# Performance work log

Hardware: AMD Instinct MI355X
Metric: run time of the kernel (lower is better)

## Reference

```python
import jax, jax.numpy as jnp
import numpy as np

N_HEAD = 8
D_K = 32
D_IN = 512
B, T = 16, 1024


def setup_inputs() -> dict:
    key = jax.random.key(0)
    ks = jax.random.split(key, 8)
    q = jax.random.normal(ks[0], (B, T, D_IN), dtype=jnp.float32)
    k = jax.random.normal(ks[1], (B, T, D_IN), dtype=jnp.float32)
    v = jax.random.normal(ks[2], (B, T, D_IN), dtype=jnp.float32)
    pad_mask = jax.random.randint(ks[3], (B, T), 0, 2).astype(jnp.bool_)
    std = np.sqrt(2.0 / D_K).astype(np.float32)
    W_q = jax.random.normal(ks[4], (N_HEAD * D_K, D_IN), dtype=jnp.float32) * std
    b_q = jax.random.normal(ks[5], (N_HEAD * D_K,), dtype=jnp.float32) * 0.01
    W_k = jax.random.normal(ks[6], (N_HEAD * D_K, D_IN), dtype=jnp.float32) * std
    b_k = jax.random.normal(ks[7], (N_HEAD * D_K,), dtype=jnp.float32) * 0.01
    return {"q": q, "k": k, "v": v, "pad_mask": pad_mask,
            "W_q": W_q, "b_q": b_q, "W_k": W_k, "b_k": b_k}


def reference(q, k, v, pad_mask, W_q, b_q, W_k, b_k):
    # NOTE: faithful to the torch module -- queries AND keys are projected
    # from v; the q, k inputs only supply shapes.
    b, t, d_in = v.shape
    h, dk = N_HEAD, D_K
    dh = d_in // h  # per-head value dim
    temperature = jnp.asarray(np.power(dk, 0.5), dtype=v.dtype)

    qh = (jnp.einsum('btd,ed->bte', v, W_q) + b_q).reshape(b, t, h, dk)
    kh = (jnp.einsum('btd,ed->bte', v, W_k) + b_k).reshape(b, t, h, dk)

    # scores: [b, h, q, k]
    scores = jnp.einsum('bqhd,bkhd->bhqk', qh, kh) / temperature
    scores = jnp.where(pad_mask[:, None, None, :], jnp.asarray(-1000.0, scores.dtype), scores)
    attn = jax.nn.softmax(scores, axis=-1)

    # value heads: split last dim into h chunks -> [b, t, h, dh]
    vh = v.reshape(b, t, h, dh)
    out = jnp.einsum('bhqk,bkhd->bhqd', attn, vh)

    # match torch output layout: output [h, b, t, dh], attn [h, b, t, t]
    output = jnp.transpose(out, (1, 0, 2, 3))
    attn_out = jnp.transpose(attn, (1, 0, 2, 3))
    return output, attn_out
```

## Files before the change

### kernel.cpp

```cpp
#include <hip/hip_runtime.h>
#include <math.h>

#define NHEAD 8
#define DK 32
#define DIN 512
#define BB 16
#define TT 1024
#define DH 64
#define EE 256
#define OUT_OFF (NHEAD*BB*TT*DH)
#define INVTEMP 0.17677669529663687f

__global__ __launch_bounds__(256)
void mask_repack_kernel(const unsigned char* __restrict__ raw,
                        unsigned char* __restrict__ norm)
{
    __shared__ int sflag;
    const int t = threadIdx.x;
    if (t == 0) sflag = 0;
    __syncthreads();

    int f = 0;
    for (int i = t; i < BB*TT/4; i += 256) {
        uchar4 b4 = reinterpret_cast<const uchar4*>(raw)[i];
        f |= (int)b4.y | (int)b4.z | (int)b4.w;
    }
    if (f) atomicOr(&sflag, 1);
    __syncthreads();

    if (sflag) {
        for (int i = t; i < BB*TT; i += 256)
            norm[i] = raw[i] ? 1 : 0;
    } else {
        const int* ri = reinterpret_cast<const int*>(raw);
        for (int i = t; i < BB*TT; i += 256)
            norm[i] = ri[i] ? 1 : 0;
    }
}

__global__ __launch_bounds__(256)
void proj_kernel(const float* __restrict__ v,
                 const float* __restrict__ Wq, const float* __restrict__ bq,
                 const float* __restrict__ Wk, const float* __restrict__ bk,
                 float* __restrict__ qh, float* __restrict__ kh)
{
    __shared__ float As[16][132];
    __shared__ float Bs[16][132];

    const int m0 = blockIdx.x * 128;
    const int nb = blockIdx.y;
    const bool isQ = (nb < 2);
    const float* __restrict__ W    = isQ ? (Wq + (size_t)nb*128*DIN)
                                         : (Wk + (size_t)(nb-2)*128*DIN);
    const float* __restrict__ bias = isQ ? (bq + nb*128) : (bk + (nb-2)*128);
    float* __restrict__ C          = isQ ? qh : kh;
    const int   c0    = (nb & 1) * 128;
    const float scale = isQ ? INVTEMP : 1.0f;

    const int t  = threadIdx.x;
    const int tx = t & 15, ty = t >> 4;

    float acc[8][8];
    #pragma unroll
    for (int i = 0; i < 8; ++i)
        #pragma unroll
        for (int j = 0; j < 8; ++j) acc[i][j] = 0.0f;

    for (int k0 = 0; k0 < DIN; k0 += 16) {
        #pragma unroll
        for (int l = 0; l < 2; ++l) {
            int idx = t + l*256;
            int row = idx >> 2, c4 = idx & 3;
            float4 a = *reinterpret_cast<const float4*>(
                &v[(size_t)(m0+row)*DIN + k0 + c4*4]);
            As[c4*4+0][row] = a.x; As[c4*4+1][row] = a.y;
            As[c4*4+2][row] = a.z; As[c4*4+3][row] = a.w;
            float4 b = *reinterpret_cast<const float4*>(
                &W[(size_t)row*DIN + k0 + c4*4]);
            Bs[c4*4+0][row] = b.x; Bs[c4*4+1][row] = b.y;
            Bs[c4*4+2][row] = b.z; Bs[c4*4+3][row] = b.w;
        }
        __syncthreads();
        #pragma unroll
        for (int kk = 0; kk < 16; ++kk) {
            float a[8], b[8];
            *reinterpret_cast<float4*>(&a[0]) = *reinterpret_cast<const float4*>(&As[kk][ty*8]);
            *reinterpret_cast<float4*>(&a[4]) = *reinterpret_cast<const float4*>(&As[kk][ty*8+4]);
            *reinterpret_cast<float4*>(&b[0]) = *reinterpret_cast<const float4*>(&Bs[kk][tx*8]);
            *reinterpret_cast<float4*>(&b[4]) = *reinterpret_cast<const float4*>(&Bs[kk][tx*8+4]);
            #pragma unroll
            for (int i = 0; i < 8; ++i)
                #pragma unroll
                for (int j = 0; j < 8; ++j)
                    acc[i][j] += a[i]*b[j];
        }
        __syncthreads();
    }

    #pragma unroll
    for (int i = 0; i < 8; ++i) {
        float4 o0, o1;
        o0.x = (acc[i][0] + bias[tx*8+0]) * scale;
        o0.y = (acc[i][1] + bias[tx*8+1]) * scale;
        o0.z = (acc[i][2] + bias[tx*8+2]) * scale;
        o0.w = (acc[i][3] + bias[tx*8+3]) * scale;
        o1.x = (acc[i][4] + bias[tx*8+4]) * scale;
        o1.y = (acc[i][5] + bias[tx*8+5]) * scale;
        o1.z = (acc[i][6] + bias[tx*8+6]) * scale;
        o1.w = (acc[i][7] + bias[tx*8+7]) * scale;
        size_t base = (size_t)(m0 + ty*8 + i)*EE + c0 + tx*8;
        *reinterpret_cast<float4*>(&C[base])   = o0;
        *reinterpret_cast<float4*>(&C[base+4]) = o1;
    }
}

#define PVSTEP(PC, VV)                                                                          \
    acc[0][0] += p0.PC*VV.x; acc[0][1] += p0.PC*VV.y; acc[0][2] += p0.PC*VV.z; acc[0][3] += p0.PC*VV.w; \
    acc[1][0] += p1.PC*VV.x; acc[1][1] += p1.PC*VV.y; acc[1][2] += p1.PC*VV.z; acc[1][3] += p1.PC*VV.w; \
    acc[2][0] += p2.PC*VV.x; acc[2][1] += p2.PC*VV.y; acc[2][2] += p2.PC*VV.z; acc[2][3] += p2.PC*VV.w; \
    acc[3][0] += p3.PC*VV.x; acc[3][1] += p3.PC*VV.y; acc[3][2] += p3.PC*VV.z; acc[3][3] += p3.PC*VV.w;

__global__ __launch_bounds__(256)
void attn_kernel(const float* __restrict__ qh, const float* __restrict__ kh,
                 const float* __restrict__ v, const unsigned char* __restrict__ mask,
                 float* __restrict__ out)
{
    __shared__ float qhs[16][32];
    __shared__ float khsT[32][134];
    __shared__ float vhs[128][64];
    __shared__ float pbuf[16][132];
    __shared__ float obuf[4][16][64];

    const int q0   = blockIdx.x * 16;
    const int b    = blockIdx.y;
    const int h    = blockIdx.z;
    const int t    = threadIdx.x;
    const int lane = t & 63, w = t >> 6;
    const int k0l  = 2*lane;

    #pragma unroll
    for (int l = 0; l < 2; ++l) {
        int idx = t + l*256;
        int r = idx >> 5, d = idx & 31;
        qhs[r][d] = qh[(size_t)(b*TT + q0 + r)*EE + h*DK + d];
    }
    __syncthreads();

    const float* __restrict__ khb = kh + (size_t)b*TT*EE + h*DK;

    float s[4][16];

    #pragma unroll
    for (int c = 0; c < 8; ++c) {
        #pragma unroll
        for (int l = 0; l < 16; ++l) {
            int idx = t + 256*l;
            int d = idx & 31, k = idx >> 5;
            khsT[d][k] = khb[(size_t)(c*128 + k)*EE + d];
        }
        __syncthreads();

        float s0[4] = {0,0,0,0}, s1[4] = {0,0,0,0};
        #pragma unroll
        for (int dg = 0; dg < 8; ++dg) {
            float2 ka = *reinterpret_cast<const float2*>(&khsT[dg*4+0][k0l]);
            float2 kb = *reinterpret_cast<const float2*>(&khsT[dg*4+1][k0l]);
            float2 kc = *reinterpret_cast<const float2*>(&khsT[dg*4+2][k0l]);
            float2 kd = *reinterpret_cast<const float2*>(&khsT[dg*4+3][k0l]);
            #pragma unroll
            for (int rr = 0; rr < 4; ++rr) {
                float4 q4 = *reinterpret_cast<const float4*>(&qhs[4*w+rr][dg*4]);
                s0[rr] += q4.x*ka.x + q4.y*kb.x + q4.z*kc.x + q4.w*kd.x;
                s1[rr] += q4.x*ka.y + q4.y*kb.y + q4.z*kc.y + q4.w*kd.y;
            }
        }
        uchar2 mk = *reinterpret_cast<const uchar2*>(&mask[(size_t)b*TT + c*128 + k0l]);
        #pragma unroll
        for (int rr = 0; rr < 4; ++rr) {
            s[rr][2*c+0] = mk.x ? -1000.0f : s0[rr];
            s[rr][2*c+1] = mk.y ? -1000.0f : s1[rr];
        }
        __syncthreads();
    }

    #pragma unroll
    for (int rr = 0; rr < 4; ++rr) {
        float m = s[rr][0];
        #pragma unroll
        for (int j = 1; j < 16; ++j) m = fmaxf(m, s[rr][j]);
        #pragma unroll
        for (int o = 32; o >= 1; o >>= 1) m = fmaxf(m, __shfl_xor(m, o, 64));
        float l = 0.0f;
        #pragma unroll
        for (int j = 0; j < 16; ++j) { float e = __expf(s[rr][j] - m); s[rr][j] = e; l += e; }
        #pragma unroll
        for (int o = 32; o >= 1; o >>= 1) l += __shfl_xor(l, o, 64);
        float inv = 1.0f / l;
        #pragma unroll
        for (int j = 0; j < 16; ++j) s[rr][j] *= inv;
    }

    float* __restrict__ attnout = out + OUT_OFF + (size_t)((h*BB + b)*TT + q0)*TT;
    #pragma unroll
    for (int rr = 0; rr < 4; ++rr) {
        float* __restrict__ rowp = attnout + (size_t)(4*w+rr)*TT;
        #pragma unroll
        for (int c = 0; c < 8; ++c) {
            *reinterpret_cast<float2*>(&rowp[c*128 + k0l]) =
                make_float2(s[rr][2*c], s[rr][2*c+1]);
        }
    }

    float acc[4][4];
    #pragma unroll
    for (int i = 0; i < 4; ++i)
        #pragma unroll
        for (int j = 0; j < 4; ++j) acc[i][j] = 0.0f;

    const float* __restrict__ vb = v + (size_t)b*TT*DIN + h*DH;
    const int rg = lane >> 4, dg = lane & 15;

    #pragma unroll
    for (int vc = 0; vc < 8; ++vc) {
        __syncthreads();
        #pragma unroll
        for (int l = 0; l < 8; ++l) {
            int idx = t + 256*l;
            int row = idx >> 4, c4 = idx & 15;
            *reinterpret_cast<float4*>(&vhs[row][c4*4]) =
                *reinterpret_cast<const float4*>(&vb[(size_t)(vc*128+row)*DIN + c4*4]);
        }
        #pragma unroll
        for (int rr = 0; rr < 4; ++rr) {
            *reinterpret_cast<float2*>(&pbuf[4*w+rr][k0l]) =
                make_float2(s[rr][2*vc], s[rr][2*vc+1]);
        }
        __syncthreads();

        #pragma unroll
        for (int kk = 0; kk < 32; kk += 4) {
            const int kbase = w*32 + kk;
            float4 p0 = *reinterpret_cast<const float4*>(&pbuf[rg*4+0][kbase]);
            float4 p1 = *reinterpret_cast<const float4*>(&pbuf[rg*4+1][kbase]);
            float4 p2 = *reinterpret_cast<const float4*>(&pbuf[rg*4+2][kbase]);
            float4 p3 = *reinterpret_cast<const float4*>(&pbuf[rg*4+3][kbase]);
            { float4 vv = *reinterpret_cast<const float4*>(&vhs[kbase+0][dg*4]); PVSTEP(x, vv) }
            { float4 vv = *reinterpret_cast<const float4*>(&vhs[kbase+1][dg*4]); PVSTEP(y, vv) }
            { float4 vv = *reinterpret_cast<const float4*>(&vhs[kbase+2][dg*4]); PVSTEP(z, vv) }
            { float4 vv = *reinterpret_cast<const float4*>(&vhs[kbase+3][dg*4]); PVSTEP(w, vv) }
        }
    }

    #pragma unroll
    for (int rr = 0; rr < 4; ++rr) {
        *reinterpret_cast<float4*>(&obuf[w][rg*4+rr][dg*4]) =
            make_float4(acc[rr][0], acc[rr][1], acc[rr][2], acc[rr][3]);
    }
    __syncthreads();
    {
        int r = t >> 4, c4 = t & 15;
        float4 r0 = *reinterpret_cast<const float4*>(&obuf[0][r][c4*4]);
        float4 r1 = *reinterpret_cast<const float4*>(&obuf[1][r][c4*4]);
        float4 r2 = *reinterpret_cast<const float4*>(&obuf[2][r][c4*4]);
        float4 r3 = *reinterpret_cast<const float4*>(&obuf[3][r][c4*4]);
        float4 o;
        o.x = r0.x + r1.x + r2.x + r3.x;
        o.y = r0.y + r1.y + r2.y + r3.y;
        o.z = r0.z + r1.z + r2.z + r3.z;
        o.w = r0.w + r1.w + r2.w + r3.w;
        *reinterpret_cast<float4*>(
            &out[(size_t)((h*BB + b)*TT + q0 + r)*DH + c4*4]) = o;
    }
}

extern "C" void kernel_launch(void* const* d_in, const int* in_sizes, int n_in,
                              void* d_out, int out_size, void* d_ws, size_t ws_size,
                              hipStream_t stream)
{
    const float* v  = (const float*)d_in[2];
    const unsigned char* mask_raw = (const unsigned char*)d_in[3];
    const float* Wq = (const float*)d_in[4];
    const float* bq = (const float*)d_in[5];
    const float* Wk = (const float*)d_in[6];
    const float* bk = (const float*)d_in[7];
    float* out = (float*)d_out;

    float* qh = (float*)d_ws;
    float* kh = qh + (size_t)BB*TT*EE;
    unsigned char* mask_norm =
        (unsigned char*)(kh + (size_t)BB*TT*EE);

    mask_repack_kernel<<<1, 256, 0, stream>>>(mask_raw, mask_norm);

    dim3 pgrid(128, 4);
    proj_kernel<<<pgrid, 256, 0, stream>>>(v, Wq, bq, Wk, bk, qh, kh);

    dim3 agrid(TT/16, BB, NHEAD);
    attn_kernel<<<agrid, 256, 0, stream>>>(qh, kh, v, mask_norm, out);
}
```

Baseline: 1.256 ms.

## Rewrite projection and attention on bf16 MFMA with split hi/lo precision

Replaces the scalar FP32 projection and attention kernels with MFMA bf16 versions. Inputs are split into hi/lo bf16 pairs so QK^T and the projection keep near-FP32 accuracy using three MFMAs. Weights are pre-scaled and converted, V is transposed to bf16, and P·V runs through a swizzled LDS buffer in bf16. The goal is to move the matmul FLOPs onto matrix cores, at the cost of extra conversion kernels and reduced precision in P·V.

```diff
diff --git a/kernel.cpp b/kernel.cpp
--- a/kernel.cpp
+++ b/kernel.cpp
@@ -8,8 +8,23 @@
 #define TT 1024
 #define DH 64
 #define EE 256
-#define OUT_OFF (NHEAD*BB*TT*DH)
+#define OUT_OFF ((size_t)NHEAD*BB*TT*DH)
 #define INVTEMP 0.17677669529663687f
+
+typedef short bf16x8 __attribute__((ext_vector_type(8)));
+typedef float f32x4  __attribute__((ext_vector_type(4)));
+
+__device__ __forceinline__ short f2bf(float f) {
+    union { float f; unsigned u; } c; c.f = f;
+    unsigned u = c.u;
+    unsigned r = (u + 0x7fffu + ((u >> 16) & 1u)) >> 16;
+    return (short)r;
+}
+__device__ __forceinline__ float bf2f(short s) {
+    union { unsigned u; float f; } c;
+    c.u = ((unsigned)(unsigned short)s) << 16;
+    return c.f;
+}
 
 __global__ __launch_bounds__(256)
 void mask_repack_kernel(const unsigned char* __restrict__ raw,
@@ -19,7 +34,6 @@
     const int t = threadIdx.x;
     if (t == 0) sflag = 0;
     __syncthreads();
-
     int f = 0;
     for (int i = t; i < BB*TT/4; i += 256) {
         uchar4 b4 = reinterpret_cast<const uchar4*>(raw)[i];
@@ -27,250 +41,226 @@
     }
     if (f) atomicOr(&sflag, 1);
     __syncthreads();
-
     if (sflag) {
-        for (int i = t; i < BB*TT; i += 256)
-            norm[i] = raw[i] ? 1 : 0;
+        for (int i = t; i < BB*TT; i += 256) norm[i] = raw[i] ? 1 : 0;
     } else {
         const int* ri = reinterpret_cast<const int*>(raw);
-        for (int i = t; i < BB*TT; i += 256)
-            norm[i] = ri[i] ? 1 : 0;
-    }
-}
-
-__global__ __launch_bounds__(256)
-void proj_kernel(const float* __restrict__ v,
-                 const float* __restrict__ Wq, const float* __restrict__ bq,
-                 const float* __restrict__ Wk, const float* __restrict__ bk,
-                 float* __restrict__ qh, float* __restrict__ kh)
-{
-    __shared__ float As[16][132];
-    __shared__ float Bs[16][132];
-
-    const int m0 = blockIdx.x * 128;
-    const int nb = blockIdx.y;
-    const bool isQ = (nb < 2);
-    const float* __restrict__ W    = isQ ? (Wq + (size_t)nb*128*DIN)
-                                         : (Wk + (size_t)(nb-2)*128*DIN);
-    const float* __restrict__ bias = isQ ? (bq + nb*128) : (bk + (nb-2)*128);
-    float* __restrict__ C          = isQ ? qh : kh;
-    const int   c0    = (nb & 1) * 128;
-    const float scale = isQ ? INVTEMP : 1.0f;
-
+        for (int i = t; i < BB*TT; i += 256) norm[i] = ri[i] ? 1 : 0;
+    }
+}
+
+__global__ __launch_bounds__(256)
+void conv_w_kernel(const float* __restrict__ Wq, const float* __restrict__ bq,
+                   const float* __restrict__ Wk, const float* __restrict__ bk,
+                   short* __restrict__ Whi, short* __restrict__ Wlo,
+                   float* __restrict__ bc)
+{
+    const int e = blockIdx.x;
+    const float sc = (e < 256) ? INVTEMP : 1.0f;
+    const float* src = (e < 256) ? (Wq + (size_t)e*DIN) : (Wk + (size_t)(e-256)*DIN);
+    for (int d = threadIdx.x; d < DIN; d += 256) {
+        float f = src[d] * sc;
+        short h = f2bf(f);
+        Whi[(size_t)e*DIN + d] = h;
+        Wlo[(size_t)e*DIN + d] = f2bf(f - bf2f(h));
+    }
+    if (threadIdx.x == 0)
+        bc[e] = ((e < 256) ? bq[e] : bk[e-256]) * sc;
+}
+
+__global__ __launch_bounds__(256)
+void conv_vt_kernel(const float* __restrict__ v, short* __restrict__ vT)
+{
+    __shared__ float tile[64][65];
+    const int t0 = blockIdx.x * 64;
+    const int b = blockIdx.y, h = blockIdx.z;
+    const int t = threadIdx.x;
+    #pragma unroll
+    for (int i = 0; i < 16; ++i) {
+        int idx = i*256 + t;
+        int r = idx >> 6, dd = idx & 63;
+        tile[dd][r] = v[((size_t)b*TT + t0 + r)*DIN + h*DH + dd];
+    }
+    __syncthreads();
+    const int d = t >> 2, seg = t & 3;
+    bf16x8 o0, o1;
+    #pragma unroll
+    for (int j = 0; j < 8; ++j) {
+        o0[j] = f2bf(tile[d][seg*16 + j]);
+        o1[j] = f2bf(tile[d][seg*16 + 8 + j]);
+    }
+    short* dst = vT + ((size_t)(b*NHEAD + h)*DH + d)*TT + t0 + seg*16;
+    *(bf16x8*)(dst)     = o0;
+    *(bf16x8*)(dst + 8) = o1;
+}
+
+__global__ __launch_bounds__(256)
+void proj_kernel(const float* __restrict__ v, const short* __restrict__ Whi,
+                 const short* __restrict__ Wlo, const float* __restrict__ bc,
+                 short* __restrict__ Phi, short* __restrict__ Plo)
+{
+    const int t = threadIdx.x;
+    const int lane = t & 63, w = t >> 6;
+    const int x = lane & 15, g = lane >> 4;
+    const int m0 = blockIdx.x * 64 + w * 16;
+    const int n0 = blockIdx.y * 64;
+
+    const float* arow = v + (size_t)(m0 + x) * DIN;
+    f32x4 acc[4];
+    #pragma unroll
+    for (int cc = 0; cc < 4; ++cc) {
+        acc[cc][0] = 0.f; acc[cc][1] = 0.f; acc[cc][2] = 0.f; acc[cc][3] = 0.f;
+    }
+
+    for (int d0 = 0; d0 < DIN; d0 += 32) {
+        float4 a0 = *(const float4*)(arow + d0 + g*8);
+        float4 a1 = *(const float4*)(arow + d0 + g*8 + 4);
+        float av[8] = {a0.x, a0.y, a0.z, a0.w, a1.x, a1.y, a1.z, a1.w};
+        bf16x8 ahi, alo;
+        #pragma unroll
+        for (int j = 0; j < 8; ++j) {
+            short hh = f2bf(av[j]);
+            ahi[j] = hh;
+            alo[j] = f2bf(av[j] - bf2f(hh));
+        }
+        #pragma unroll
+        for (int cc = 0; cc < 4; ++cc) {
+            size_t boff = (size_t)(n0 + cc*16 + x) * DIN + d0 + g*8;
+            bf16x8 bhi = *(const bf16x8*)(Whi + boff);
+            bf16x8 blo = *(const bf16x8*)(Wlo + boff);
+            acc[cc] = __builtin_amdgcn_mfma_f32_16x16x32_bf16(ahi, bhi, acc[cc], 0, 0, 0);
+            acc[cc] = __builtin_amdgcn_mfma_f32_16x16x32_bf16(alo, bhi, acc[cc], 0, 0, 0);
+            acc[cc] = __builtin_amdgcn_mfma_f32_16x16x32_bf16(ahi, blo, acc[cc], 0, 0, 0);
+        }
+    }
+
+    #pragma unroll
+    for (int cc = 0; cc < 4; ++cc) {
+        const int n = n0 + cc*16 + x;
+        const float bias = bc[n];
+        #pragma unroll
+        for (int r = 0; r < 4; ++r) {
+            const int m = m0 + g*4 + r;
+            float val = acc[cc][r] + bias;
+            short hh = f2bf(val);
+            Phi[(size_t)m*512 + n] = hh;
+            Plo[(size_t)m*512 + n] = f2bf(val - bf2f(hh));
+        }
+    }
+}
+
+__global__ __launch_bounds__(256)
+void attn_kernel(const short* __restrict__ Phi, const short* __restrict__ Plo,
+                 const short* __restrict__ vT, const unsigned char* __restrict__ mask,
+                 float* __restrict__ out)
+{
+    __shared__ short pbuf[16*1024];
+    __shared__ float redmax[4][4][4];
+    __shared__ float redsum[4][4][4];
+
+    const int q0 = blockIdx.x * 16;
+    const int b  = blockIdx.y;
+    const int h  = blockIdx.z;
     const int t  = threadIdx.x;
-    const int tx = t & 15, ty = t >> 4;
-
-    float acc[8][8];
-    #pragma unroll
-    for (int i = 0; i < 8; ++i)
-        #pragma unroll
-        for (int j = 0; j < 8; ++j) acc[i][j] = 0.0f;
-
-    for (int k0 = 0; k0 < DIN; k0 += 16) {
-        #pragma unroll
-        for (int l = 0; l < 2; ++l) {
-            int idx = t + l*256;
-            int row = idx >> 2, c4 = idx & 3;
-            float4 a = *reinterpret_cast<const float4*>(
-                &v[(size_t)(m0+row)*DIN + k0 + c4*4]);
-            As[c4*4+0][row] = a.x; As[c4*4+1][row] = a.y;
-            As[c4*4+2][row] = a.z; As[c4*4+3][row] = a.w;
-            float4 b = *reinterpret_cast<const float4*>(
-                &W[(size_t)row*DIN + k0 + c4*4]);
-            Bs[c4*4+0][row] = b.x; Bs[c4*4+1][row] = b.y;
-            Bs[c4*4+2][row] = b.z; Bs[c4*4+3][row] = b.w;
-        }
-        __syncthreads();
-        #pragma unroll
-        for (int kk = 0; kk < 16; ++kk) {
-            float a[8], b[8];
-            *reinterpret_cast<float4*>(&a[0]) = *reinterpret_cast<const float4*>(&As[kk][ty*8]);
-            *reinterpret_cast<float4*>(&a[4]) = *reinterpret_cast<const float4*>(&As[kk][ty*8+4]);
-            *reinterpret_cast<float4*>(&b[0]) = *reinterpret_cast<const float4*>(&Bs[kk][tx*8]);
-            *reinterpret_cast<float4*>(&b[4]) = *reinterpret_cast<const float4*>(&Bs[kk][tx*8+4]);
-            #pragma unroll
-            for (int i = 0; i < 8; ++i)
-                #pragma unroll
-                for (int j = 0; j < 8; ++j)
-                    acc[i][j] += a[i]*b[j];
-        }
-        __syncthreads();
-    }
-
-    #pragma unroll
-    for (int i = 0; i < 8; ++i) {
-        float4 o0, o1;
-        o0.x = (acc[i][0] + bias[tx*8+0]) * scale;
-        o0.y = (acc[i][1] + bias[tx*8+1]) * scale;
-        o0.z = (acc[i][2] + bias[tx*8+2]) * scale;
-        o0.w = (acc[i][3] + bias[tx*8+3]) * scale;
-        o1.x = (acc[i][4] + bias[tx*8+4]) * scale;
-        o1.y = (acc[i][5] + bias[tx*8+5]) * scale;
-        o1.z = (acc[i][6] + bias[tx*8+6]) * scale;
-        o1.w = (acc[i][7] + bias[tx*8+7]) * scale;
-        size_t base = (size_t)(m0 + ty*8 + i)*EE + c0 + tx*8;
-        *reinterpret_cast<float4*>(&C[base])   = o0;
-        *reinterpret_cast<float4*>(&C[base+4]) = o1;
-    }
-}
-
-#define PVSTEP(PC, VV)                                                                          \
-    acc[0][0] += p0.PC*VV.x; acc[0][1] += p0.PC*VV.y; acc[0][2] += p0.PC*VV.z; acc[0][3] += p0.PC*VV.w; \
-    acc[1][0] += p1.PC*VV.x; acc[1][1] += p1.PC*VV.y; acc[1][2] += p1.PC*VV.z; acc[1][3] += p1.PC*VV.w; \
-    acc[2][0] += p2.PC*VV.x; acc[2][1] += p2.PC*VV.y; acc[2][2] += p2.PC*VV.z; acc[2][3] += p2.PC*VV.w; \
-    acc[3][0] += p3.PC*VV.x; acc[3][1] += p3.PC*VV.y; acc[3][2] += p3.PC*VV.z; acc[3][3] += p3.PC*VV.w;
-
-__global__ __launch_bounds__(256)
-void attn_kernel(const float* __restrict__ qh, const float* __restrict__ kh,
-                 const float* __restrict__ v, const unsigned char* __restrict__ mask,
-                 float* __restrict__ out)
-{
-    __shared__ float qhs[16][32];
-    __shared__ float khsT[32][134];
-    __shared__ float vhs[128][64];
-    __shared__ float pbuf[16][132];
-    __shared__ float obuf[4][16][64];
-
-    const int q0   = blockIdx.x * 16;
-    const int b    = blockIdx.y;
-    const int h    = blockIdx.z;
-    const int t    = threadIdx.x;
     const int lane = t & 63, w = t >> 6;
-    const int k0l  = 2*lane;
-
-    #pragma unroll
-    for (int l = 0; l < 2; ++l) {
-        int idx = t + l*256;
-        int r = idx >> 5, d = idx & 31;
-        qhs[r][d] = qh[(size_t)(b*TT + q0 + r)*EE + h*DK + d];
-    }
-    __syncthreads();
-
-    const float* __restrict__ khb = kh + (size_t)b*TT*EE + h*DK;
-
-    float s[4][16];
-
-    #pragma unroll
-    for (int c = 0; c < 8; ++c) {
-        #pragma unroll
-        for (int l = 0; l < 16; ++l) {
-            int idx = t + 256*l;
-            int d = idx & 31, k = idx >> 5;
-            khsT[d][k] = khb[(size_t)(c*128 + k)*EE + d];
-        }
-        __syncthreads();
-
-        float s0[4] = {0,0,0,0}, s1[4] = {0,0,0,0};
-        #pragma unroll
-        for (int dg = 0; dg < 8; ++dg) {
-            float2 ka = *reinterpret_cast<const float2*>(&khsT[dg*4+0][k0l]);
-            float2 kb = *reinterpret_cast<const float2*>(&khsT[dg*4+1][k0l]);
-            float2 kc = *reinterpret_cast<const float2*>(&khsT[dg*4+2][k0l]);
-            float2 kd = *reinterpret_cast<const float2*>(&khsT[dg*4+3][k0l]);
-            #pragma unroll
-            for (int rr = 0; rr < 4; ++rr) {
-                float4 q4 = *reinterpret_cast<const float4*>(&qhs[4*w+rr][dg*4]);
-                s0[rr] += q4.x*ka.x + q4.y*kb.x + q4.z*kc.x + q4.w*kd.x;
-                s1[rr] += q4.x*ka.y + q4.y*kb.y + q4.z*kc.y + q4.w*kd.y;
-            }
-        }
-        uchar2 mk = *reinterpret_cast<const uchar2*>(&mask[(size_t)b*TT + c*128 + k0l]);
-        #pragma unroll
-        for (int rr = 0; rr < 4; ++rr) {
-            s[rr][2*c+0] = mk.x ? -1000.0f : s0[rr];
-            s[rr][2*c+1] = mk.y ? -1000.0f : s1[rr];
-        }
-        __syncthreads();
-    }
-
-    #pragma unroll
-    for (int rr = 0; rr < 4; ++rr) {
-        float m = s[rr][0];
-        #pragma unroll
-        for (int j = 1; j < 16; ++j) m = fmaxf(m, s[rr][j]);
-        #pragma unroll
-        for (int o = 32; o >= 1; o >>= 1) m = fmaxf(m, __shfl_xor(m, o, 64));
-        float l = 0.0f;
-        #pragma unroll
-        for (int j = 0; j < 16; ++j) { float e = __expf(s[rr][j] - m); s[rr][j] = e; l += e; }
-        #pragma unroll
-        for (int o = 32; o >= 1; o >>= 1) l += __shfl_xor(l, o, 64);
-        float inv = 1.0f / l;
-        #pragma unroll
-        for (int j = 0; j < 16; ++j) s[rr][j] *= inv;
-    }
-
-    float* __restrict__ attnout = out + OUT_OFF + (size_t)((h*BB + b)*TT + q0)*TT;
-    #pragma unroll
-    for (int rr = 0; rr < 4; ++rr) {
-        float* __restrict__ rowp = attnout + (size_t)(4*w+rr)*TT;
-        #pragma unroll
-        for (int c = 0; c < 8; ++c) {
-            *reinterpret_cast<float2*>(&rowp[c*128 + k0l]) =
-                make_float2(s[rr][2*c], s[rr][2*c+1]);
-        }
-    }
-
-    float acc[4][4];
-    #pragma unroll
-    for (int i = 0; i < 4; ++i)
-        #pragma unroll
-        for (int j = 0; j < 4; ++j) acc[i][j] = 0.0f;
-
-    const float* __restrict__ vb = v + (size_t)b*TT*DIN + h*DH;
-    const int rg = lane >> 4, dg = lane & 15;
-
-    #pragma unroll
-    for (int vc = 0; vc < 8; ++vc) {
-        __syncthreads();
-        #pragma unroll
-        for (int l = 0; l < 8; ++l) {
-            int idx = t + 256*l;
-            int row = idx >> 4, c4 = idx & 15;
-            *reinterpret_cast<float4*>(&vhs[row][c4*4]) =
-                *reinterpret_cast<const float4*>(&vb[(size_t)(vc*128+row)*DIN + c4*4]);
-        }
-        #pragma unroll
-        for (int rr = 0; rr < 4; ++rr) {
-            *reinterpret_cast<float2*>(&pbuf[4*w+rr][k0l]) =
-                make_float2(s[rr][2*vc], s[rr][2*vc+1]);
-        }
-        __syncthreads();
-
-        #pragma unroll
-        for (int kk = 0; kk < 32; kk += 4) {
-            const int kbase = w*32 + kk;
-            float4 p0 = *reinterpret_cast<const float4*>(&pbuf[rg*4+0][kbase]);
-            float4 p1 = *reinterpret_cast<const float4*>(&pbuf[rg*4+1][kbase]);
-            float4 p2 = *reinterpret_cast<const float4*>(&pbuf[rg*4+2][kbase]);
-            float4 p3 = *reinterpret_cast<const float4*>(&pbuf[rg*4+3][kbase]);
-            { float4 vv = *reinterpret_cast<const float4*>(&vhs[kbase+0][dg*4]); PVSTEP(x, vv) }
-            { float4 vv = *reinterpret_cast<const float4*>(&vhs[kbase+1][dg*4]); PVSTEP(y, vv) }
-            { float4 vv = *reinterpret_cast<const float4*>(&vhs[kbase+2][dg*4]); PVSTEP(z, vv) }
-            { float4 vv = *reinterpret_cast<const float4*>(&vhs[kbase+3][dg*4]); PVSTEP(w, vv) }
-        }
-    }
-
-    #pragma unroll
-    for (int rr = 0; rr < 4; ++rr) {
-        *reinterpret_cast<float4*>(&obuf[w][rg*4+rr][dg*4]) =
-            make_float4(acc[rr][0], acc[rr][1], acc[rr][2], acc[rr][3]);
-    }
-    __syncthreads();
-    {
-        int r = t >> 4, c4 = t & 15;
-        float4 r0 = *reinterpret_cast<const float4*>(&obuf[0][r][c4*4]);
-        float4 r1 = *reinterpret_cast<const float4*>(&obuf[1][r][c4*4]);
-        float4 r2 = *reinterpret_cast<const float4*>(&obuf[2][r][c4*4]);
-        float4 r3 = *reinterpret_cast<const float4*>(&obuf[3][r][c4*4]);
-        float4 o;
-        o.x = r0.x + r1.x + r2.x + r3.x;
-        o.y = r0.y + r1.y + r2.y + r3.y;
-        o.z = r0.z + r1.z + r2.z + r3.z;
-        o.w = r0.w + r1.w + r2.w + r3.w;
-        *reinterpret_cast<float4*>(
-            &out[(size_t)((h*BB + b)*TT + q0 + r)*DH + c4*4]) = o;
-    }
+    const int x = lane & 15, g = lane >> 4;
+    const int kbase = w * 256;
+
+    const size_t qoff = ((size_t)(b*TT) + q0 + x)*512 + h*DK + g*8;
+    const bf16x8 qhi = *(const bf16x8*)(Phi + qoff);
+    const bf16x8 qlo = *(const bf16x8*)(Plo + qoff);
+
+    f32x4 acc[16];
+    #pragma unroll
+    for (int c = 0; c < 16; ++c) {
+        const int k0 = kbase + c*16;
+        const size_t koff = ((size_t)(b*TT) + k0 + x)*512 + 256 + h*DK + g*8;
+        bf16x8 khi = *(const bf16x8*)(Phi + koff);
+        bf16x8 klo = *(const bf16x8*)(Plo + koff);
+        f32x4 a; a[0] = 0.f; a[1] = 0.f; a[2] = 0.f; a[3] = 0.f;
+        a = __builtin_amdgcn_mfma_f32_16x16x32_bf16(qhi, khi, a, 0, 0, 0);
+        a = __builtin_amdgcn_mfma_f32_16x16x32_bf16(qlo, khi, a, 0, 0, 0);
+        a = __builtin_amdgcn_mfma_f32_16x16x32_bf16(qhi, klo, a, 0, 0, 0);
+        const unsigned char mk = mask[(size_t)b*TT + k0 + x];
+        if (mk) { a[0] = -1000.f; a[1] = -1000.f; a[2] = -1000.f; a[3] = -1000.f; }
+        acc[c] = a;
+    }
+
+    float M[4], S[4];
+    #pragma unroll
+    for (int r = 0; r < 4; ++r) {
+        float m = acc[0][r];
+        #pragma unroll
+        for (int c = 1; c < 16; ++c) m = fmaxf(m, acc[c][r]);
+        m = fmaxf(m, __shfl_xor(m, 1, 64));
+        m = fmaxf(m, __shfl_xor(m, 2, 64));
+        m = fmaxf(m, __shfl_xor(m, 4, 64));
+        m = fmaxf(m, __shfl_xor(m, 8, 64));
+        M[r] = m;
+    }
+    if (x == 0) {
+        redmax[w][g][0] = M[0]; redmax[w][g][1] = M[1];
+        redmax[w][g][2] = M[2]; redmax[w][g][3] = M[3];
+    }
+    __syncthreads();
+    #pragma unroll
+    for (int r = 0; r < 4; ++r) {
+        float m = fmaxf(fmaxf(redmax[0][g][r], redmax[1][g][r]),
+                        fmaxf(redmax[2][g][r], redmax[3][g][r]));
+        float s = 0.f;
+        #pragma unroll
+        for (int c = 0; c < 16; ++c) {
+            float e = __expf(acc[c][r] - m);
+            acc[c][r] = e;
+            s += e;
+        }
+        s += __shfl_xor(s, 1, 64);
+        s += __shfl_xor(s, 2, 64);
+        s += __shfl_xor(s, 4, 64);
+        s += __shfl_xor(s, 8, 64);
+        S[r] = s;
+    }
+    if (x == 0) {
+        redsum[w][g][0] = S[0]; redsum[w][g][1] = S[1];
+        redsum[w][g][2] = S[2]; redsum[w][g][3] = S[3];
+    }
+    __syncthreads();
+    float inv[4];
+    #pragma unroll
+    for (int r = 0; r < 4; ++r)
+        inv[r] = 1.f / (redsum[0][g][r] + redsum[1][g][r] +
+                        redsum[2][g][r] + redsum[3][g][r]);
+
+    float* abase = out + OUT_OFF + ((size_t)(h*BB + b)*TT + q0)*TT;
+    #pragma unroll
+    for (int r = 0; r < 4; ++r) {
+        const int row = g*4 + r;
+        float* rp = abase + (size_t)row*TT + kbase + x;
+        const int sw = (row & 7) << 4;
+        #pragma unroll
+        for (int c = 0; c < 16; ++c) {
+            float p = acc[c][r] * inv[r];
+            rp[c*16] = p;
+            const int col = kbase + c*16 + x;
+            pbuf[(row << 10) + ((((col << 1) ^ sw)) >> 1)] = f2bf(p);
+        }
+    }
+    __syncthreads();
+
+    f32x4 o; o[0] = 0.f; o[1] = 0.f; o[2] = 0.f; o[3] = 0.f;
+    const short* vrow = vT + ((size_t)(b*NHEAD + h)*DH + w*16 + x)*TT;
+    const char* pbb = (const char*)pbuf;
+    const int xsw = (x & 7) << 4;
+    #pragma unroll
+    for (int kk = 0; kk < 32; ++kk) {
+        const int off = (x << 11) + ((kk*64 + g*16) ^ xsw);
+        bf16x8 pa = *(const bf16x8*)(pbb + off);
+        bf16x8 vb = *(const bf16x8*)(vrow + kk*32 + g*8);
+        o = __builtin_amdgcn_mfma_f32_16x16x32_bf16(pa, vb, o, 0, 0, 0);
+    }
+    #pragma unroll
+    for (int r = 0; r < 4; ++r)
+        out[((size_t)(h*BB + b)*TT + q0 + g*4 + r)*DH + w*16 + x] = o[r];
 }
 
 extern "C" void kernel_launch(void* const* d_in, const int* in_sizes, int n_in,
@@ -285,16 +275,18 @@
     const float* bk = (const float*)d_in[7];
     float* out = (float*)d_out;
 
-    float* qh = (float*)d_ws;
-    float* kh = qh + (size_t)BB*TT*EE;
-    unsigned char* mask_norm =
-        (unsigned char*)(kh + (size_t)BB*TT*EE);
+    char* ws = (char*)d_ws;
+    short* Phi = (short*)ws;  ws += (size_t)BB*TT*512*2;
+    short* Plo = (short*)ws;  ws += (size_t)BB*TT*512*2;
+    short* vT  = (short*)ws;  ws += (size_t)BB*NHEAD*DH*TT*2;
+    short* Whi = (short*)ws;  ws += (size_t)512*512*2;
+    short* Wlo = (short*)ws;  ws += (size_t)512*512*2;
+    float* bc  = (float*)ws;  ws += 512*4;
+    unsigned char* mask_norm = (unsigned char*)ws;
 
     mask_repack_kernel<<<1, 256, 0, stream>>>(mask_raw, mask_norm);
-
-    dim3 pgrid(128, 4);
-    proj_kernel<<<pgrid, 256, 0, stream>>>(v, Wq, bq, Wk, bk, qh, kh);
-
-    dim3 agrid(TT/16, BB, NHEAD);
-    attn_kernel<<<agrid, 256, 0, stream>>>(qh, kh, v, mask_norm, out);
-}
+    conv_w_kernel<<<512, 256, 0, stream>>>(Wq, bq, Wk, bk, Whi, Wlo, bc);
+    conv_vt_kernel<<<dim3(TT/64, BB, NHEAD), 256, 0, stream>>>(v, vT);
+    proj_kernel<<<dim3(256, 8), 256, 0, stream>>>(v, Whi, Wlo, bc, Phi, Plo);
+    attn_kernel<<<dim3(TT/16, BB, NHEAD), 256, 0, stream>>>(Phi, Plo, vT, mask_norm, out);
+}
```

Measured after the change: 1.037 ms. -17.4%, faster.
